# Optimization experiments

Measured on AMD Instinct MI355X. Metric: run time of the kernel, lower is better.

Reference implementation:

```python
import jax, jax.numpy as jnp
import numpy as np

B, S, D = 2, 2048, 1024
H, DH = 16, 64  # H*DH == D


def setup_inputs() -> dict:
    key = jax.random.key(0)
    ks = jax.random.split(key, 7)
    scale = 1.0 / np.sqrt(D)
    return {
        "x": jax.random.normal(ks[0], (B, S, D), dtype=jnp.float32),
        "mask": jax.random.normal(ks[1], (B, 1, 1, S), dtype=jnp.float32),
        "Wq": jax.random.normal(ks[2], (D, D), dtype=jnp.float32) * scale,
        "Wk": jax.random.normal(ks[3], (D, D), dtype=jnp.float32) * scale,
        "Wv": jax.random.normal(ks[4], (D, D), dtype=jnp.float32) * scale,
        "Wo": jax.random.normal(ks[5], (D, D), dtype=jnp.float32) * scale,
        "bo": jax.random.normal(ks[6], (D,), dtype=jnp.float32) * 0.01,
    }


def reference(x, mask, Wq, Wk, Wv, Wo, bo):
    # QKV projections (bias-free), split heads: [B,S,D] -> [B,H,S,DH]
    def split_heads(t):
        return t.reshape(B, S, H, DH).transpose(0, 2, 1, 3)

    q = split_heads(x @ Wq)
    k = split_heads(x @ Wk)
    v = split_heads(x @ Wv)

    # NOTE: module scales by sqrt(input_dim), not sqrt(head_size)
    scores = jnp.einsum("bhqd,bhkd->bhqk", q, k) / jnp.sqrt(jnp.float32(D))
    scores = scores + mask  # additive mask, broadcast [B,1,1,S]
    attn = jax.nn.softmax(scores, axis=-1)
    ctx = jnp.einsum("bhqk,bhkd->bhqd", attn, v)  # [B,H,S,DH]
    ctx = ctx.transpose(0, 2, 1, 3).reshape(B, S, H * DH)
    return ctx @ Wo + bo
```

## Files before the change

### kernel.cpp

```cpp
#include <hip/hip_runtime.h>
#include <hip/hip_bf16.h>

#define BB 2
#define SS 2048
#define DD 1024
#define HH 16
#define DHD 64
#define QKLD 2048

typedef __attribute__((ext_vector_type(8))) __bf16 bf16x8;
typedef __attribute__((ext_vector_type(4))) __bf16 bf16x4;
typedef __attribute__((ext_vector_type(4))) float f32x4;
typedef __attribute__((ext_vector_type(16))) float f32x16;

__device__ __forceinline__ f32x4 mfma16(bf16x8 a, bf16x8 b, f32x4 c) {
  return __builtin_amdgcn_mfma_f32_16x16x32_bf16(a, b, c, 0, 0, 0);
}
__device__ __forceinline__ f32x16 mfma32(bf16x8 a, bf16x8 b, f32x16 c) {
  return __builtin_amdgcn_mfma_f32_32x32x16_bf16(a, b, c, 0, 0, 0);
}
__device__ __forceinline__ void gload_lds16(const void* g, void* l) {
  __builtin_amdgcn_global_load_lds((__attribute__((address_space(1))) const void*)g,
                                   (__attribute__((address_space(3))) void*)l, 16, 0, 0);
}
__device__ __forceinline__ f32x16 zero16() {
  f32x16 z;
#pragma unroll
  for (int i = 0; i < 16; ++i) z[i] = 0.f;
  return z;
}
__device__ __forceinline__ bf16x8 frag4(unsigned a, unsigned b, unsigned c, unsigned d) {
  union { unsigned u[4]; bf16x8 v; } x;
  x.u[0] = a; x.u[1] = b; x.u[2] = c; x.u[3] = d;
  return x.v;
}
__device__ __forceinline__ unsigned pack2(float lo, float hi) {
  union { __bf16 h[2]; unsigned u; } x;
  x.h[0] = (__bf16)lo; x.h[1] = (__bf16)hi;
  return x.u;
}

__global__ __launch_bounds__(256) void prep_kernel(
    const float* __restrict__ x, __bf16* __restrict__ xb,
    const float* __restrict__ mask, __bf16* __restrict__ embf,
    const float* __restrict__ Wq, const float* __restrict__ Wk,
    const float* __restrict__ Wv, const float* __restrict__ Wo,
    __bf16* __restrict__ WTbase) {
  __shared__ __bf16 t[64][65];
  int id = blockIdx.x, tid = threadIdx.x;
  if (id < 4096) {
    int i = id * 256 + tid;
    float4 f = ((const float4*)x)[i];
    bf16x4 o;
    o[0] = (__bf16)f.x; o[1] = (__bf16)f.y; o[2] = (__bf16)f.z; o[3] = (__bf16)f.w;
    *(bf16x4*)(xb + (size_t)i * 4) = o;
    return;
  }
  if (id < 4112) {
    int j = (id - 4096) * 256 + tid;
    embf[j] = (__bf16)__expf(mask[j]);
    return;
  }
  int idx = id - 4112;
  int z = idx >> 8, rem = idx & 255;
  const float* W = (z == 0) ? Wq : (z == 1) ? Wk : (z == 2) ? Wv : Wo;
  __bf16* WT = WTbase + ((size_t)z << 20);
  int c0 = (rem & 15) * 64, r0 = (rem >> 4) * 64;
  {
    int rr = tid >> 4, cg = tid & 15;
#pragma unroll
    for (int it = 0; it < 4; ++it) {
      int r = rr + it * 16;
      float4 f = *(const float4*)(W + (size_t)(r0 + r) * DD + c0 + cg * 4);
      t[r][cg * 4 + 0] = (__bf16)f.x;
      t[r][cg * 4 + 1] = (__bf16)f.y;
      t[r][cg * 4 + 2] = (__bf16)f.z;
      t[r][cg * 4 + 3] = (__bf16)f.w;
    }
  }
  __syncthreads();
  {
    int sg = tid & 7;
#pragma unroll
    for (int it = 0; it < 2; ++it) {
      int wc = (tid >> 3) + it * 32;
      __bf16 tmp[8];
#pragma unroll
      for (int e = 0; e < 8; ++e) tmp[e] = t[sg * 8 + e][wc];
      bf16x8 o;
#pragma unroll
      for (int e = 0; e < 8; ++e) o[e] = tmp[e];
      *(bf16x8*)(WT + (size_t)(c0 + wc) * DD + r0 + sg * 8) = o;
    }
  }
}

template <int MODE>
__device__ __forceinline__ void gemm_body(
    char* AsB, char* BsB, int bx, int by,
    const __bf16* __restrict__ A, const __bf16* __restrict__ BT,
    float* __restrict__ Cf, __bf16* __restrict__ Cb,
    const float* __restrict__ bias, const __bf16* __restrict__ embf,
    int M, int N, int K) {
  int tid = threadIdx.x;
  int lane = tid & 63, wave = tid >> 6;
  int lr = lane & 15, lg = lane >> 4;
  int wr = wave >> 1, wc = wave & 1;
  int m0 = bx * 128, n0 = by * 128;

  int o0 = wave * 1024 + lane * 16;
  int r0i = o0 >> 6, s0i = ((o0 >> 4) & 3) ^ (r0i & 3);
  int o1 = o0 + 4096;
  int r1i = o1 >> 6, s1i = ((o1 >> 4) & 3) ^ (r1i & 3);

  const __bf16* Ag0 = A + (size_t)(m0 + r0i) * K + s0i * 8;
  const __bf16* Ag1 = A + (size_t)(m0 + r1i) * K + s1i * 8;
  const __bf16* Bg0 = BT + (size_t)(n0 + r0i) * K + s0i * 8;
  const __bf16* Bg1 = BT + (size_t)(n0 + r1i) * K + s1i * 8;
  int lb0 = wave * 1024, lb1 = wave * 1024 + 4096;

  f32x4 acc[4][4];
#pragma unroll
  for (int m = 0; m < 4; ++m)
#pragma unroll
    for (int n = 0; n < 4; ++n) acc[m][n] = (f32x4){0.f, 0.f, 0.f, 0.f};

  gload_lds16(Ag0, AsB + lb0);
  gload_lds16(Ag1, AsB + lb1);
  gload_lds16(Bg0, BsB + lb0);
  gload_lds16(Bg1, BsB + lb1);
  __syncthreads();

  int NK = K >> 5;
  for (int it = 0; it < NK; ++it) {
    int cur = it & 1;
    if (it + 1 < NK) {
      int ko = (it + 1) * 32;
      char* An = AsB + (cur ^ 1) * 8192;
      char* Bn = BsB + (cur ^ 1) * 8192;
      gload_lds16(Ag0 + ko, An + lb0);
      gload_lds16(Ag1 + ko, An + lb1);
      gload_lds16(Bg0 + ko, Bn + lb0);
      gload_lds16(Bg1 + ko, Bn + lb1);
    }
    const char* Ab = AsB + cur * 8192;
    const char* Bb = BsB + cur * 8192;
    bf16x8 af[4], bfr[4];
#pragma unroll
    for (int m = 0; m < 4; ++m) {
      int row = wr * 64 + m * 16 + lr;
      af[m] = *(const bf16x8*)(Ab + row * 64 + ((lg ^ (row & 3)) << 4));
    }
#pragma unroll
    for (int n = 0; n < 4; ++n) {
      int row = wc * 64 + n * 16 + lr;
      bfr[n] = *(const bf16x8*)(Bb + row * 64 + ((lg ^ (row & 3)) << 4));
    }
#pragma unroll
    for (int m = 0; m < 4; ++m)
#pragma unroll
      for (int n = 0; n < 4; ++n) acc[m][n] = mfma16(af[m], bfr[n], acc[m][n]);
    __syncthreads();
  }

#pragma unroll
  for (int m = 0; m < 4; ++m) {
#pragma unroll
    for (int n = 0; n < 4; ++n) {
      int cc = n0 + wc * 64 + n * 16 + lr;
      float ef = 0.f;
      if constexpr (MODE == 2) ef = (float)embf[cc];
#pragma unroll
      for (int r = 0; r < 4; ++r) {
        int rr = m0 + wr * 64 + m * 16 + 4 * lg + r;
        if constexpr (MODE == 1) {
          Cf[(size_t)rr * N + cc] = acc[m][n][r] + bias[cc];
        } else if constexpr (MODE == 0) {
          Cb[(size_t)rr * N + cc] = (__bf16)acc[m][n][r];
        } else {
          int bb2 = cc >> 11, sl = cc & (SS - 1);
          int hh = rr >> 6, dd2 = rr & 63;
          Cb[(((size_t)bb2 * HH + hh) * DHD + dd2) * SS + sl] =
              (__bf16)(acc[m][n][r] * ef);
        }
      }
    }
  }
}

__global__ __launch_bounds__(256, 2) void proj_kernel(
    const __bf16* __restrict__ xb, const __bf16* __restrict__ WqT,
    const __bf16* __restrict__ WvT, __bf16* __restrict__ qkb,
    __bf16* __restrict__ vtb, const __bf16* __restrict__ embf) {
  __shared__ __bf16 As[2][128 * 32];
  __shared__ __bf16 Bs[2][128 * 32];
  int id = blockIdx.x;
  if (id < 512) {
    gemm_body<0>((char*)As, (char*)Bs, id & 31, id >> 5,
                 xb, WqT, nullptr, qkb, nullptr, nullptr, 4096, 2048, 1024);
  } else {
    int i2 = id - 512;
    gemm_body<2>((char*)As, (char*)Bs, i2 & 7, i2 >> 3,
                 WvT, xb, nullptr, vtb, nullptr, embf, 1024, 4096, 1024);
  }
}

__global__ __launch_bounds__(256, 2) void ogemm_kernel(
    const __bf16* __restrict__ ctxb, const __bf16* __restrict__ WoT,
    float* __restrict__ out, const float* __restrict__ bo) {
  __shared__ __bf16 As[2][128 * 32];
  __shared__ __bf16 Bs[2][128 * 32];
  gemm_body<1>((char*)As, (char*)Bs, blockIdx.x, blockIdx.y,
               ctxb, WoT, out, nullptr, bo, nullptr, 4096, 1024, 1024);
}

__global__ __launch_bounds__(256, 2) void attn_kernel(
    const __bf16* __restrict__ QK, const __bf16* __restrict__ VT,
    const __bf16* __restrict__ embf, __bf16* __restrict__ ctxb) {
  __shared__ __bf16 Ks[2][64 * 64];
  __shared__ __bf16 Vs[2][64 * 64];

  int h = blockIdx.y, b = blockIdx.z;
  int tid = threadIdx.x;
  int wave = tid >> 6, lane = tid & 63;
  int l31 = lane & 31, hi = lane >> 5;
  int rx = l31 & 7;

  int q0 = blockIdx.x * 128 + wave * 32;
  const __bf16* qp = QK + ((size_t)(b * SS) + q0 + l31) * QKLD + h * DHD + 8 * hi;
  bf16x8 qfrag[4];
#pragma unroll
  for (int kc = 0; kc < 4; ++kc) qfrag[kc] = *(const bf16x8*)(qp + 16 * kc);

  int o0 = tid * 16;
  int row0 = o0 >> 7;
  int ss0 = ((o0 >> 4) & 7) ^ (row0 & 7);
  int lw0 = wave * 1024, lw1 = wave * 1024 + 4096;

  const __bf16* kg = QK + (size_t)(b * SS) * QKLD + DD + h * DHD;
  const __bf16* vg = VT + ((size_t)(b * HH + h) * DHD) * SS;
  const __bf16* Kg0 = kg + (size_t)row0 * QKLD + ss0 * 8;
  const __bf16* Kg1 = kg + (size_t)(row0 + 32) * QKLD + ss0 * 8;
  const __bf16* Vg0 = vg + (size_t)row0 * SS + ss0 * 8;
  const __bf16* Vg1 = vg + (size_t)(row0 + 32) * SS + ss0 * 8;
  const __bf16* ep = embf + b * SS + 8 * hi;

  gload_lds16(Kg0, (char*)Ks[0] + lw0);
  gload_lds16(Kg1, (char*)Ks[0] + lw1);
  gload_lds16(Vg0, (char*)Vs[0] + lw0);
  gload_lds16(Vg1, (char*)Vs[0] + lw1);

  f32x16 ctx0 = zero16(), ctx1 = zero16(), lacc = zero16();
  const float SCALE = 0.03125f;
  __syncthreads();

  const int NT = SS / 64;
  for (int it = 0; it < NT; ++it) {
    int cur = it & 1;
    int kb = it * 64;
    if (it + 1 < NT) {
      size_t ko = (size_t)(it + 1) * 64 * QKLD;
      int vo = (it + 1) * 64;
      gload_lds16(Kg0 + ko, (char*)Ks[cur ^ 1] + lw0);
      gload_lds16(Kg1 + ko, (char*)Ks[cur ^ 1] + lw1);
      gload_lds16(Vg0 + vo, (char*)Vs[cur ^ 1] + lw0);
      gload_lds16(Vg1 + vo, (char*)Vs[cur ^ 1] + lw1);
    }
    bf16x8 emf[4];
#pragma unroll
    for (int q2 = 0; q2 < 4; ++q2) emf[q2] = *(const bf16x8*)(ep + kb + 16 * q2);

    const char* Kb = (const char*)Ks[cur];
    const char* Vb = (const char*)Vs[cur];
#pragma unroll
    for (int kc32 = 0; kc32 < 2; ++kc32) {
      f32x16 sc = zero16();
#pragma unroll
      for (int kc = 0; kc < 4; ++kc) {
        bf16x8 kf = *(const bf16x8*)(Kb + (kc32 * 32 + l31) * 128 +
                                     ((((kc << 1) + hi) ^ rx) << 4));
        sc = mfma32(kf, qfrag[kc], sc);
      }
      unsigned pk[8];
#pragma unroll
      for (int i2 = 0; i2 < 8; ++i2)
        pk[i2] = pack2(__expf(sc[2 * i2] * SCALE), __expf(sc[2 * i2 + 1] * SCALE));
      unsigned sx0 = __shfl_xor(pk[0], 32, 64);
      unsigned sx1 = __shfl_xor(pk[1], 32, 64);
      unsigned sx2 = __shfl_xor(pk[2], 32, 64);
      unsigned sx3 = __shfl_xor(pk[3], 32, 64);
      unsigned sx4 = __shfl_xor(pk[4], 32, 64);
      unsigned sx5 = __shfl_xor(pk[5], 32, 64);
      unsigned sx6 = __shfl_xor(pk[6], 32, 64);
      unsigned sx7 = __shfl_xor(pk[7], 32, 64);
      unsigned w0 = hi ? sx2 : pk[0];
      unsigned w1 = hi ? sx3 : pk[1];
      unsigned w2 = hi ? pk[2] : sx0;
      unsigned w3 = hi ? pk[3] : sx1;
      unsigned w4 = hi ? sx6 : pk[4];
      unsigned w5 = hi ? sx7 : pk[5];
      unsigned w6 = hi ? pk[6] : sx4;
      unsigned w7 = hi ? pk[7] : sx5;
      bf16x8 pf0 = frag4(w0, w1, w2, w3);
      bf16x8 pf1 = frag4(w4, w5, w6, w7);
      lacc = mfma32(pf0, emf[kc32 * 2 + 0], lacc);
      lacc = mfma32(pf1, emf[kc32 * 2 + 1], lacc);
      {
        bf16x8 v00 = *(const bf16x8*)(Vb + (l31)*128 + ((((kc32 << 2) + 0 + hi) ^ rx) << 4));
        ctx0 = mfma32(pf0, v00, ctx0);
        bf16x8 v01 = *(const bf16x8*)(Vb + (l31)*128 + ((((kc32 << 2) + 2 + hi) ^ rx) << 4));
        ctx0 = mfma32(pf1, v01, ctx0);
        bf16x8 v10 = *(const bf16x8*)(Vb + (32 + l31) * 128 + ((((kc32 << 2) + 0 + hi) ^ rx) << 4));
        ctx1 = mfma32(pf0, v10, ctx1);
        bf16x8 v11 = *(const bf16x8*)(Vb + (32 + l31) * 128 + ((((kc32 << 2) + 2 + hi) ^ rx) << 4));
        ctx1 = mfma32(pf1, v11, ctx1);
      }
    }
    __syncthreads();
  }
#pragma unroll
  for (int i = 0; i < 16; ++i) {
    float inv = 1.0f / lacc[i];
    int q = (i & 3) + 8 * (i >> 2) + 4 * hi;
    __bf16* op = ctxb + ((size_t)(b * SS) + q0 + q) * DD + h * DHD + l31;
    op[0] = (__bf16)(ctx0[i] * inv);
    op[32] = (__bf16)(ctx1[i] * inv);
  }
}

extern "C" void kernel_launch(void* const* d_in, const int* in_sizes, int n_in,
                              void* d_out, int out_size, void* d_ws, size_t ws_size,
                              hipStream_t stream) {
  const float* x    = (const float*)d_in[0];
  const float* mask = (const float*)d_in[1];
  const float* Wq   = (const float*)d_in[2];
  const float* Wk   = (const float*)d_in[3];
  const float* Wv   = (const float*)d_in[4];
  const float* Wo   = (const float*)d_in[5];
  const float* bo   = (const float*)d_in[6];
  float* out = (float*)d_out;

  char* ws = (char*)d_ws;
  const size_t MB = 1024 * 1024;
  __bf16* xb   = (__bf16*)(ws + 0);
  __bf16* WqT  = (__bf16*)(ws + 8 * MB);
  __bf16* WvT  = (__bf16*)(ws + 12 * MB);
  __bf16* WoT  = (__bf16*)(ws + 14 * MB);
  __bf16* qkb  = (__bf16*)(ws + 16 * MB);
  __bf16* vtb  = (__bf16*)(ws + 32 * MB);
  __bf16* embf = (__bf16*)(ws + 40 * MB);
  __bf16* ctxb = xb;

  prep_kernel<<<5136, 256, 0, stream>>>(x, xb, mask, embf, Wq, Wk, Wv, Wo, WqT);
  proj_kernel<<<768, 256, 0, stream>>>(xb, WqT, WvT, qkb, vtb, embf);
  attn_kernel<<<dim3(16, HH, BB), 256, 0, stream>>>(qkb, vtb, embf, ctxb);
  ogemm_kernel<<<dim3(32, 8), 256, 0, stream>>>(ctxb, WoT, out, bo);
}
```

Baseline: 208.9 us.

## Rebalance thread-block sizes for attention and output GEMM kernels

Attention blocks shrink from 4 to 2 waves, each covering 64 query rows, which doubles the grid to 1024 blocks for better CU fill. Each thread now issues four K and four V LDS loads per tile instead of two. The output GEMM becomes a dedicated 512-thread kernel with 8 waves in a 2x4 layout, each wave computing a 64x32 subtile with 16x16 MFMAs. The projection kernel's launch bound rises to 3 blocks per SM; the cost is less K/V tile reuse per block and more register pressure.

Result: no change. 211.3 us (+1.2%).

```diff
diff --git a/kernel.cpp b/kernel.cpp
--- a/kernel.cpp
+++ b/kernel.cpp
@@ -188,7 +188,7 @@
   }
 }
 
-__global__ __launch_bounds__(256, 2) void proj_kernel(
+__global__ __launch_bounds__(256, 3) void proj_kernel(
     const __bf16* __restrict__ xb, const __bf16* __restrict__ WqT,
     const __bf16* __restrict__ WvT, __bf16* __restrict__ qkb,
     __bf16* __restrict__ vtb, const __bf16* __restrict__ embf) {
@@ -205,16 +205,78 @@
   }
 }
 
-__global__ __launch_bounds__(256, 2) void ogemm_kernel(
+__global__ __launch_bounds__(512, 2) void ogemm_kernel(
     const __bf16* __restrict__ ctxb, const __bf16* __restrict__ WoT,
     float* __restrict__ out, const float* __restrict__ bo) {
   __shared__ __bf16 As[2][128 * 32];
   __shared__ __bf16 Bs[2][128 * 32];
-  gemm_body<1>((char*)As, (char*)Bs, blockIdx.x, blockIdx.y,
-               ctxb, WoT, out, nullptr, bo, nullptr, 4096, 1024, 1024);
-}
-
-__global__ __launch_bounds__(256, 2) void attn_kernel(
+  const int K = 1024, N = 1024;
+  int tid = threadIdx.x;
+  int lane = tid & 63, wave = tid >> 6;
+  int lr = lane & 15, lg = lane >> 4;
+  int wr = wave >> 2, wc = wave & 3;
+  int m0 = blockIdx.x * 128, n0 = blockIdx.y * 128;
+
+  int o0 = tid * 16;
+  int row0 = o0 >> 6;
+  int s0i = ((o0 >> 4) & 3) ^ (row0 & 3);
+  const __bf16* Ag = ctxb + (size_t)(m0 + row0) * K + s0i * 8;
+  const __bf16* Bg = WoT + (size_t)(n0 + row0) * K + s0i * 8;
+  int lb = wave * 1024;
+
+  f32x4 acc[4][2];
+#pragma unroll
+  for (int m = 0; m < 4; ++m)
+#pragma unroll
+    for (int n = 0; n < 2; ++n) acc[m][n] = (f32x4){0.f, 0.f, 0.f, 0.f};
+
+  gload_lds16(Ag, (char*)As[0] + lb);
+  gload_lds16(Bg, (char*)Bs[0] + lb);
+  __syncthreads();
+
+  const int NK = K >> 5;
+  for (int it = 0; it < NK; ++it) {
+    int cur = it & 1;
+    if (it + 1 < NK) {
+      int ko = (it + 1) * 32;
+      gload_lds16(Ag + ko, (char*)As[cur ^ 1] + lb);
+      gload_lds16(Bg + ko, (char*)Bs[cur ^ 1] + lb);
+    }
+    const char* Ab = (const char*)As[cur];
+    const char* Bb = (const char*)Bs[cur];
+    bf16x8 af[4], bfr[2];
+#pragma unroll
+    for (int m = 0; m < 4; ++m) {
+      int row = wr * 64 + m * 16 + lr;
+      af[m] = *(const bf16x8*)(Ab + row * 64 + ((lg ^ (row & 3)) << 4));
+    }
+#pragma unroll
+    for (int n = 0; n < 2; ++n) {
+      int row = wc * 32 + n * 16 + lr;
+      bfr[n] = *(const bf16x8*)(Bb + row * 64 + ((lg ^ (row & 3)) << 4));
+    }
+#pragma unroll
+    for (int m = 0; m < 4; ++m)
+#pragma unroll
+      for (int n = 0; n < 2; ++n) acc[m][n] = mfma16(af[m], bfr[n], acc[m][n]);
+    __syncthreads();
+  }
+
+#pragma unroll
+  for (int m = 0; m < 4; ++m) {
+#pragma unroll
+    for (int n = 0; n < 2; ++n) {
+      int cc = n0 + wc * 32 + n * 16 + lr;
+#pragma unroll
+      for (int r = 0; r < 4; ++r) {
+        int rr = m0 + wr * 64 + m * 16 + 4 * lg + r;
+        out[(size_t)rr * N + cc] = acc[m][n][r] + bo[cc];
+      }
+    }
+  }
+}
+
+__global__ __launch_bounds__(128, 2) void attn_kernel(
     const __bf16* __restrict__ QK, const __bf16* __restrict__ VT,
     const __bf16* __restrict__ embf, __bf16* __restrict__ ctxb) {
   __shared__ __bf16 Ks[2][64 * 64];
@@ -226,29 +288,32 @@
   int l31 = lane & 31, hi = lane >> 5;
   int rx = l31 & 7;
 
-  int q0 = blockIdx.x * 128 + wave * 32;
+  int q0 = blockIdx.x * 64 + wave * 32;
   const __bf16* qp = QK + ((size_t)(b * SS) + q0 + l31) * QKLD + h * DHD + 8 * hi;
   bf16x8 qfrag[4];
 #pragma unroll
   for (int kc = 0; kc < 4; ++kc) qfrag[kc] = *(const bf16x8*)(qp + 16 * kc);
 
-  int o0 = tid * 16;
-  int row0 = o0 >> 7;
-  int ss0 = ((o0 >> 4) & 7) ^ (row0 & 7);
-  int lw0 = wave * 1024, lw1 = wave * 1024 + 4096;
+  int row0 = tid >> 3;
+  int ss0 = (tid & 7) ^ ((tid >> 3) & 7);
+  int lwb = wave * 1024;
 
   const __bf16* kg = QK + (size_t)(b * SS) * QKLD + DD + h * DHD;
   const __bf16* vg = VT + ((size_t)(b * HH + h) * DHD) * SS;
-  const __bf16* Kg0 = kg + (size_t)row0 * QKLD + ss0 * 8;
-  const __bf16* Kg1 = kg + (size_t)(row0 + 32) * QKLD + ss0 * 8;
-  const __bf16* Vg0 = vg + (size_t)row0 * SS + ss0 * 8;
-  const __bf16* Vg1 = vg + (size_t)(row0 + 32) * SS + ss0 * 8;
+  const __bf16* Kgj[4];
+  const __bf16* Vgj[4];
+#pragma unroll
+  for (int j = 0; j < 4; ++j) {
+    Kgj[j] = kg + (size_t)(row0 + 16 * j) * QKLD + ss0 * 8;
+    Vgj[j] = vg + (size_t)(row0 + 16 * j) * SS + ss0 * 8;
+  }
   const __bf16* ep = embf + b * SS + 8 * hi;
 
-  gload_lds16(Kg0, (char*)Ks[0] + lw0);
-  gload_lds16(Kg1, (char*)Ks[0] + lw1);
-  gload_lds16(Vg0, (char*)Vs[0] + lw0);
-  gload_lds16(Vg1, (char*)Vs[0] + lw1);
+#pragma unroll
+  for (int j = 0; j < 4; ++j) {
+    gload_lds16(Kgj[j], (char*)Ks[0] + j * 2048 + lwb);
+    gload_lds16(Vgj[j], (char*)Vs[0] + j * 2048 + lwb);
+  }
 
   f32x16 ctx0 = zero16(), ctx1 = zero16(), lacc = zero16();
   const float SCALE = 0.03125f;
@@ -261,10 +326,11 @@
     if (it + 1 < NT) {
       size_t ko = (size_t)(it + 1) * 64 * QKLD;
       int vo = (it + 1) * 64;
-      gload_lds16(Kg0 + ko, (char*)Ks[cur ^ 1] + lw0);
-      gload_lds16(Kg1 + ko, (char*)Ks[cur ^ 1] + lw1);
-      gload_lds16(Vg0 + vo, (char*)Vs[cur ^ 1] + lw0);
-      gload_lds16(Vg1 + vo, (char*)Vs[cur ^ 1] + lw1);
+#pragma unroll
+      for (int j = 0; j < 4; ++j) {
+        gload_lds16(Kgj[j] + ko, (char*)Ks[cur ^ 1] + j * 2048 + lwb);
+        gload_lds16(Vgj[j] + vo, (char*)Vs[cur ^ 1] + j * 2048 + lwb);
+      }
     }
     bf16x8 emf[4];
 #pragma unroll
@@ -353,6 +419,6 @@
 
   prep_kernel<<<5136, 256, 0, stream>>>(x, xb, mask, embf, Wq, Wk, Wv, Wo, WqT);
   proj_kernel<<<768, 256, 0, stream>>>(xb, WqT, WvT, qkb, vtb, embf);
-  attn_kernel<<<dim3(16, HH, BB), 256, 0, stream>>>(qkb, vtb, embf, ctxb);
-  ogemm_kernel<<<dim3(32, 8), 256, 0, stream>>>(ctxb, WoT, out, bo);
-}
+  attn_kernel<<<dim3(SS / 64, HH, BB), 128, 0, stream>>>(qkb, vtb, embf, ctxb);
+  ogemm_kernel<<<dim3(32, 8), 512, 0, stream>>>(ctxb, WoT, out, bo);
+}
```
